# Optimization experiments

Measured on AMD Instinct MI355X. Metric: run time of the kernel, lower is better.

The kernel has to match this reference:

```python
import jax, jax.numpy as jnp
import numpy as np

N_HEAD = 16


def setup_inputs() -> dict:
    key = jax.random.key(0)
    k1, k2, k3 = jax.random.split(key, 3)
    B, T, C = 4, 1024, 1024
    x = jax.random.normal(k1, (B, T, C), dtype=jnp.float32)
    w_attn = jax.random.normal(k2, (3 * C, C), dtype=jnp.float32) * 0.02
    w_proj = jax.random.normal(k3, (C, C), dtype=jnp.float32) * 0.02
    return {"x": x, "w_attn": w_attn, "w_proj": w_proj}


def reference(x, w_attn, w_proj):
    B, T, C = x.shape
    H = N_HEAD
    hs = C // H
    scale = 1.0 / np.sqrt(hs).astype(np.float32)

    qkv = x @ w_attn.T                         # [B, T, 3C]
    q, k, v = jnp.split(qkv, 3, axis=-1)
    q = q.reshape(B, T, H, hs).transpose(0, 2, 1, 3)   # [B, H, T, hs]
    k = k.reshape(B, T, H, hs).transpose(0, 2, 1, 3)
    v = v.reshape(B, T, H, hs).transpose(0, 2, 1, 3)

    scores = jnp.einsum('bhqd,bhkd->bhqk', q, k) * scale   # [B, H, T, T]
    causal = jnp.tril(jnp.ones((T, T), dtype=bool))
    scores = jnp.where(causal, scores, -jnp.inf)

    att = jax.nn.sigmoid(scores)                # sigmoid attention, not softmax
    # Bernoulli straight-through sampling (value = sample, grad flows via att)
    samp_key = jax.random.fold_in(jax.random.key(0), 42)
    samples = jax.random.bernoulli(samp_key, att).astype(att.dtype)
    att = att + jax.lax.stop_gradient(samples - att)

    y = jnp.einsum('bhqk,bhkd->bhqd', att, v)   # [B, H, T, hs]
    att_sum = att.sum(axis=-1)                  # [B, H, T]
    att_var = (att * (1.0 - att)).sum(axis=-1)  # [B, H, T]

    y = y.transpose(0, 2, 1, 3).reshape(B, T, C)
    y = y @ w_proj.T
    return (y, att_sum, att_var)
```

## Files before the change

kernel.cpp:

```cpp
#include <hip/hip_runtime.h>
#include <stdint.h>


#define T_SEQ 1024
#define QKV_LD 3072

typedef __attribute__((ext_vector_type(8))) short bf16x8;
typedef __attribute__((ext_vector_type(4))) float f32x4;
typedef __attribute__((ext_vector_type(4))) unsigned int u32x4;

typedef __attribute__((address_space(3))) uint32_t lds_u32;
typedef __attribute__((address_space(1))) const uint32_t g_u32;

#define ROTL(x, d) __builtin_amdgcn_alignbit((x), (x), 32 - (d))

__device__ __forceinline__ void threefry2x32(uint32_t k0, uint32_t k1,
                                             uint32_t x0, uint32_t x1,
                                             uint32_t &o0, uint32_t &o1) {
  uint32_t ks2 = k0 ^ k1 ^ 0x1BD11BDAu;
#define TF_R4(a, b, c, d)                                                      \
  x0 += x1; x1 = ROTL(x1, a); x1 ^= x0;                                        \
  x0 += x1; x1 = ROTL(x1, b); x1 ^= x0;                                        \
  x0 += x1; x1 = ROTL(x1, c); x1 ^= x0;                                        \
  x0 += x1; x1 = ROTL(x1, d); x1 ^= x0;
  x0 += k0; x1 += k1;
  TF_R4(13, 15, 26, 6)
  x0 += k1; x1 += ks2 + 1u;
  TF_R4(17, 29, 16, 24)
  x0 += ks2; x1 += k0 + 2u;
  TF_R4(13, 15, 26, 6)
  x0 += k0; x1 += k1 + 3u;
  TF_R4(17, 29, 16, 24)
  x0 += k1; x1 += ks2 + 4u;
  TF_R4(13, 15, 26, 6)
  x0 += ks2; x1 += k0 + 5u;
  o0 = x0; o1 = x1;
#undef TF_R4
}

__device__ __forceinline__ unsigned short f2bf(float f) {
  uint32_t u = __float_as_uint(f);
  u += 0x7FFFu + ((u >> 16) & 1u);
  return (unsigned short)(u >> 16);
}

#define N_X4  1048576
#define N_WA4 786432
#define N_WP4 262144

__global__ __launch_bounds__(256) void cvt3_bf16(const float4* __restrict__ x,
                                                 const float4* __restrict__ wa,
                                                 const float4* __restrict__ wp,
                                                 uint2* __restrict__ out) {
  size_t i = (size_t)blockIdx.x * 256 + threadIdx.x;
  const float4* src;
  size_t off;
  if (i < N_X4) { src = x; off = i; }
  else if (i < N_X4 + N_WA4) { src = wa; off = i - N_X4; }
  else { src = wp; off = i - (N_X4 + N_WA4); }
  float4 v = src[off];
  uint2 o;
  o.x = (uint32_t)f2bf(v.x) | ((uint32_t)f2bf(v.y) << 16);
  o.y = (uint32_t)f2bf(v.z) | ((uint32_t)f2bf(v.w) << 16);
  out[i] = o;
}

template <int OUT_BF16>
__global__ __launch_bounds__(256) void gemm_bf16(const unsigned short* __restrict__ A,
                                                 const unsigned short* __restrict__ B,
                                                 void* __restrict__ Cout,
                                                 int M, int N, int K) {
  __shared__ unsigned short As[128 * 32];
  __shared__ unsigned short Bs[128 * 32];

  const int t = threadIdx.x;
  const int lane = t & 63, w = t >> 6;
  const int g = lane >> 4, lr = lane & 15;
  const int rw = w >> 1, cw = w & 1;
  const int bm = blockIdx.x * 128, bn = blockIdx.y * 128;

  const unsigned short* Ag = A + (size_t)(bm + 32 * w + (lane >> 2)) * K + 8 * (lane & 3);
  const unsigned short* Bg = B + (size_t)(bn + 32 * w + (lane >> 2)) * K + 8 * (lane & 3);
  lds_u32* Al0 = (lds_u32*)&As[(32 * w) * 32];
  lds_u32* Al1 = (lds_u32*)&As[(32 * w + 16) * 32];
  lds_u32* Bl0 = (lds_u32*)&Bs[(32 * w) * 32];
  lds_u32* Bl1 = (lds_u32*)&Bs[(32 * w + 16) * 32];

  f32x4 acc[4][4];
#pragma unroll
  for (int i = 0; i < 4; ++i)
#pragma unroll
    for (int j = 0; j < 4; ++j) acc[i][j] = (f32x4){0.f, 0.f, 0.f, 0.f};

  for (int k0 = 0; k0 < K; k0 += 32) {
    __syncthreads();
    __builtin_amdgcn_global_load_lds((g_u32*)(const void*)(Ag + k0), Al0, 16, 0, 0);
    __builtin_amdgcn_global_load_lds((g_u32*)(const void*)(Ag + k0 + (size_t)16 * K), Al1, 16, 0, 0);
    __builtin_amdgcn_global_load_lds((g_u32*)(const void*)(Bg + k0), Bl0, 16, 0, 0);
    __builtin_amdgcn_global_load_lds((g_u32*)(const void*)(Bg + k0 + (size_t)16 * K), Bl1, 16, 0, 0);
    __syncthreads();

    bf16x8 af[4], bfr[4];
#pragma unroll
    for (int i = 0; i < 4; ++i)
      af[i] = *(const bf16x8*)&As[(64 * rw + 16 * i + lr) * 32 + 8 * g];
#pragma unroll
    for (int j = 0; j < 4; ++j)
      bfr[j] = *(const bf16x8*)&Bs[(64 * cw + 16 * j + lr) * 32 + 8 * g];
#pragma unroll
    for (int i = 0; i < 4; ++i)
#pragma unroll
      for (int j = 0; j < 4; ++j)
        acc[i][j] = __builtin_amdgcn_mfma_f32_16x16x32_bf16(af[i], bfr[j], acc[i][j], 0, 0, 0);
  }

#pragma unroll
  for (int i = 0; i < 4; ++i)
#pragma unroll
    for (int j = 0; j < 4; ++j)
#pragma unroll
      for (int r = 0; r < 4; ++r) {
        const size_t row = bm + 64 * rw + 16 * i + 4 * g + r;
        const size_t col = bn + 64 * cw + 16 * j + lr;
        if (OUT_BF16)
          ((unsigned short*)Cout)[row * N + col] = f2bf(acc[i][j][r]);
        else
          ((float*)Cout)[row * N + col] = acc[i][j][r];
      }
}

__global__ __launch_bounds__(256) void vtrans(const unsigned short* __restrict__ qkv,
                                              unsigned short* __restrict__ Vt) {
  const int i = blockIdx.x;
  const int bh = i >> 4, kc = i & 15;
  const int b = bh >> 4, h = bh & 15;
  const int t = threadIdx.x;
  const int dr = t & 63, kgrp = t >> 6;

  const unsigned short* src =
      qkv + (size_t)(b * T_SEQ + kc * 64 + kgrp * 16) * QKV_LD + 2048 + h * 64 + dr;
  uint32_t pk[8];
#pragma unroll
  for (int j = 0; j < 8; ++j) {
    uint32_t lo = src[(size_t)(2 * j) * QKV_LD];
    uint32_t hi = src[(size_t)(2 * j + 1) * QKV_LD];
    pk[j] = lo | (hi << 16);
  }
  unsigned short* dst = Vt + ((size_t)bh * 64 + dr) * 1024 + kc * 64 + kgrp * 16;
  *(u32x4*)dst = (u32x4){pk[0], pk[1], pk[2], pk[3]};
  *(u32x4*)(dst + 8) = (u32x4){pk[4], pk[5], pk[6], pk[7]};
}

__global__ __launch_bounds__(128) void attn_nobar(const unsigned short* __restrict__ qkv,
                                                  const unsigned short* __restrict__ Vt,
                                                  unsigned short* __restrict__ yatt,
                                                  float* __restrict__ att_sum,
                                                  float* __restrict__ att_var) {
  __shared__ unsigned short St[2][16][40];

  const int t = threadIdx.x;
  const int lane = t & 63, w = t >> 6;
  const int g = lane >> 4, lr = lane & 15;
  const int i = blockIdx.x;
  const int bh = 8 * (i & 7) + ((i >> 3) & 7);
  const int p = 2 * (i >> 6) + w;
  const int b = bh >> 4, h = bh & 15;

  uint32_t dk0, dk1;
  threefry2x32(0u, 0u, 0u, 42u, dk0, dk1);

  unsigned short (*stw)[40] = St[w];
  const unsigned short* kb = qkv + (size_t)b * T_SEQ * QKV_LD + 1024 + h * 64;
  const unsigned short* vb = Vt + (size_t)bh * 64 * 1024;

#pragma unroll 1
  for (int half = 0; half < 2; ++half) {
    const int s = half ? p : 63 - p;
    const int q0 = 16 * s;
    const unsigned short* qr = qkv + (size_t)(b * T_SEQ + q0 + lr) * QKV_LD + h * 64 + 8 * g;
    const bf16x8 aq0 = *(const bf16x8*)qr;
    const bf16x8 aq1 = *(const bf16x8*)(qr + 32);

    f32x4 yacc[4];
#pragma unroll
    for (int c = 0; c < 4; ++c) yacc[c] = (f32x4){0.f, 0.f, 0.f, 0.f};
    float rs[4] = {0.f, 0.f, 0.f, 0.f};

    const int nk = (q0 + 47) >> 5;

    bf16x8 cbv[4], cbk[4];
#pragma unroll
    for (int c = 0; c < 4; ++c)
      cbv[c] = *(const bf16x8*)(vb + (size_t)(16 * c + lr) * 1024 + 8 * g);
#pragma unroll
    for (int c = 0; c < 2; ++c) {
      const unsigned short* kr = kb + (size_t)(16 * c + lr) * QKV_LD + 8 * g;
      cbk[2 * c] = *(const bf16x8*)kr;
      cbk[2 * c + 1] = *(const bf16x8*)(kr + 32);
    }

#pragma unroll 1
    for (int kt = 0; kt < nk; ++kt) {
      const int kg0 = 32 * kt;
      const int kgn = (kt + 1 < nk) ? kg0 + 32 : kg0;
      bf16x8 nbv[4], nbk[4];
#pragma unroll
      for (int c = 0; c < 4; ++c)
        nbv[c] = *(const bf16x8*)(vb + (size_t)(16 * c + lr) * 1024 + kgn + 8 * g);
#pragma unroll
      for (int c = 0; c < 2; ++c) {
        const unsigned short* kr = kb + (size_t)(kgn + 16 * c + lr) * QKV_LD + 8 * g;
        nbk[2 * c] = *(const bf16x8*)kr;
        nbk[2 * c + 1] = *(const bf16x8*)(kr + 32);
      }

#pragma unroll
      for (int c = 0; c < 2; ++c) {
        f32x4 sa = __builtin_amdgcn_mfma_f32_16x16x32_bf16(aq0, cbk[2 * c],
                                                           (f32x4){0.f, 0.f, 0.f, 0.f}, 0, 0, 0);
        sa = __builtin_amdgcn_mfma_f32_16x16x32_bf16(aq1, cbk[2 * c + 1], sa, 0, 0, 0);
        const int kg = kg0 + 16 * c + lr;
#pragma unroll
        for (int r = 0; r < 4; ++r) {
          const int qg = q0 + 4 * g + r;
          float samp = 0.f;
          if (kg <= qg) {
            float e = __expf(-0.125f * sa[r]);
            uint32_t idx = ((uint32_t)bh << 20) | ((uint32_t)qg << 10) | (uint32_t)kg;
            uint32_t r0, r1;
            threefry2x32(dk0, dk1, 0u, idx, r0, r1);
            float u = __uint_as_float(0x3F800000u | ((r0 ^ r1) >> 9)) - 1.0f;
            samp = (fmaf(u, e, u) < 1.0f) ? 1.0f : 0.0f;
          }
          rs[r] += samp;
          stw[4 * g + r][16 * c + lr] = (unsigned short)(__float_as_uint(samp) >> 16);
        }
      }

      const bf16x8 pa = *(const bf16x8*)&stw[lr][8 * g];
#pragma unroll
      for (int c = 0; c < 4; ++c)
        yacc[c] = __builtin_amdgcn_mfma_f32_16x16x32_bf16(pa, cbv[c], yacc[c], 0, 0, 0);

#pragma unroll
      for (int c = 0; c < 4; ++c) { cbv[c] = nbv[c]; cbk[c] = nbk[c]; }
    }

    const size_t yb = (size_t)(b * T_SEQ + q0) * 1024 + h * 64;
#pragma unroll
    for (int c = 0; c < 4; ++c)
#pragma unroll
      for (int r = 0; r < 4; ++r)
        yatt[yb + (size_t)(4 * g + r) * 1024 + 16 * c + lr] = f2bf(yacc[c][r]);

#pragma unroll
    for (int r = 0; r < 4; ++r) {
      rs[r] += __shfl_xor(rs[r], 1);
      rs[r] += __shfl_xor(rs[r], 2);
      rs[r] += __shfl_xor(rs[r], 4);
      rs[r] += __shfl_xor(rs[r], 8);
    }
    if (lr == 0) {
#pragma unroll
      for (int r = 0; r < 4; ++r)
        att_sum[(size_t)bh * T_SEQ + q0 + 4 * g + r] = rs[r];
    }
    if (lane < 16) att_var[(size_t)bh * T_SEQ + q0 + lane] = 0.f;
  }
}

extern "C" void kernel_launch(void* const* d_in, const int* in_sizes, int n_in,
                              void* d_out, int out_size, void* d_ws, size_t ws_size,
                              hipStream_t stream) {
  (void)in_sizes; (void)n_in; (void)out_size; (void)ws_size;
  const float* x      = (const float*)d_in[0];
  const float* w_attn = (const float*)d_in[1];
  const float* w_proj = (const float*)d_in[2];

  float* y_out      = (float*)d_out;
  float* attsum_out = y_out + (size_t)4 * 1024 * 1024;
  float* attvar_out = attsum_out + (size_t)4 * 16 * 1024;

  unsigned short* ws_us = (unsigned short*)d_ws;
  unsigned short* x_bf    = ws_us;
  unsigned short* wa_bf   = x_bf + (size_t)4 * 1024 * 1024;
  unsigned short* wp_bf   = wa_bf + (size_t)3 * 1024 * 1024;
  unsigned short* qkv_bf  = wp_bf + (size_t)1024 * 1024;
  unsigned short* yatt_bf = qkv_bf + (size_t)4096 * 3072;
  unsigned short* vt_bf   = yatt_bf + (size_t)4096 * 1024;

  dim3 blk(256);
  cvt3_bf16<<<dim3(8192), blk, 0, stream>>>((const float4*)x, (const float4*)w_attn,
                                            (const float4*)w_proj, (uint2*)x_bf);
  gemm_bf16<1><<<dim3(32, 24), blk, 0, stream>>>(x_bf, wa_bf, (void*)qkv_bf, 4096, 3072, 1024);
  vtrans<<<dim3(1024), blk, 0, stream>>>(qkv_bf, vt_bf);
  attn_nobar<<<dim3(1024), dim3(128), 0, stream>>>(qkv_bf, vt_bf, yatt_bf, attsum_out, attvar_out);
  gemm_bf16<0><<<dim3(32, 8), blk, 0, stream>>>(yatt_bf, wp_bf, (void*)y_out, 4096, 1024, 1024);
}
```

Baseline: 187.2 us.

## Give each wave one query strip in 256-thread blocks and drop register prefetch

```diff
diff --git a/kernel.cpp b/kernel.cpp
--- a/kernel.cpp
+++ b/kernel.cpp
@@ -151,20 +151,24 @@
   *(u32x4*)(dst + 8) = (u32x4){pk[4], pk[5], pk[6], pk[7]};
 }
 
-__global__ __launch_bounds__(128) void attn_nobar(const unsigned short* __restrict__ qkv,
-                                                  const unsigned short* __restrict__ Vt,
-                                                  unsigned short* __restrict__ yatt,
-                                                  float* __restrict__ att_sum,
-                                                  float* __restrict__ att_var) {
-  __shared__ unsigned short St[2][16][40];
+__global__ __launch_bounds__(256, 4) void attn_strip(const unsigned short* __restrict__ qkv,
+                                                     const unsigned short* __restrict__ Vt,
+                                                     unsigned short* __restrict__ yatt,
+                                                     float* __restrict__ att_sum,
+                                                     float* __restrict__ att_var) {
+  __shared__ unsigned short St[4][16][40];
 
   const int t = threadIdx.x;
   const int lane = t & 63, w = t >> 6;
   const int g = lane >> 4, lr = lane & 15;
   const int i = blockIdx.x;
   const int bh = 8 * (i & 7) + ((i >> 3) & 7);
-  const int p = 2 * (i >> 6) + w;
+  const int j = i >> 6;
   const int b = bh >> 4, h = bh & 15;
+
+  const int role = (w + (j >> 2)) & 3;
+  const int s = (role == 0) ? j : (role == 1) ? 63 - j : (role == 2) ? 31 - j : 32 + j;
+  const int q0 = 16 * s;
 
   uint32_t dk0, dk1;
   threefry2x32(0u, 0u, 0u, 42u, dk0, dk1);
@@ -173,100 +177,82 @@
   const unsigned short* kb = qkv + (size_t)b * T_SEQ * QKV_LD + 1024 + h * 64;
   const unsigned short* vb = Vt + (size_t)bh * 64 * 1024;
 
+  const unsigned short* qr = qkv + (size_t)(b * T_SEQ + q0 + lr) * QKV_LD + h * 64 + 8 * g;
+  const bf16x8 aq0 = *(const bf16x8*)qr;
+  const bf16x8 aq1 = *(const bf16x8*)(qr + 32);
+
+  f32x4 yacc[4];
+#pragma unroll
+  for (int c = 0; c < 4; ++c) yacc[c] = (f32x4){0.f, 0.f, 0.f, 0.f};
+  float rs[4] = {0.f, 0.f, 0.f, 0.f};
+
+  const int nk = (q0 + 47) >> 5;
+  const uint32_t lane_idx = ((uint32_t)(4 * g) << 10) | (uint32_t)lr;
+  const uint32_t base_idx = ((uint32_t)bh << 20) | ((uint32_t)q0 << 10);
+
 #pragma unroll 1
-  for (int half = 0; half < 2; ++half) {
-    const int s = half ? p : 63 - p;
-    const int q0 = 16 * s;
-    const unsigned short* qr = qkv + (size_t)(b * T_SEQ + q0 + lr) * QKV_LD + h * 64 + 8 * g;
-    const bf16x8 aq0 = *(const bf16x8*)qr;
-    const bf16x8 aq1 = *(const bf16x8*)(qr + 32);
-
-    f32x4 yacc[4];
-#pragma unroll
-    for (int c = 0; c < 4; ++c) yacc[c] = (f32x4){0.f, 0.f, 0.f, 0.f};
-    float rs[4] = {0.f, 0.f, 0.f, 0.f};
-
-    const int nk = (q0 + 47) >> 5;
-
-    bf16x8 cbv[4], cbk[4];
-#pragma unroll
-    for (int c = 0; c < 4; ++c)
-      cbv[c] = *(const bf16x8*)(vb + (size_t)(16 * c + lr) * 1024 + 8 * g);
+  for (int kt = 0; kt < nk; ++kt) {
+    const int kg0 = 32 * kt;
+    bf16x8 cbk[4], cbv[4];
 #pragma unroll
     for (int c = 0; c < 2; ++c) {
-      const unsigned short* kr = kb + (size_t)(16 * c + lr) * QKV_LD + 8 * g;
+      const unsigned short* kr = kb + (size_t)(kg0 + 16 * c + lr) * QKV_LD + 8 * g;
       cbk[2 * c] = *(const bf16x8*)kr;
       cbk[2 * c + 1] = *(const bf16x8*)(kr + 32);
     }
-
-#pragma unroll 1
-    for (int kt = 0; kt < nk; ++kt) {
-      const int kg0 = 32 * kt;
-      const int kgn = (kt + 1 < nk) ? kg0 + 32 : kg0;
-      bf16x8 nbv[4], nbk[4];
-#pragma unroll
-      for (int c = 0; c < 4; ++c)
-        nbv[c] = *(const bf16x8*)(vb + (size_t)(16 * c + lr) * 1024 + kgn + 8 * g);
-#pragma unroll
-      for (int c = 0; c < 2; ++c) {
-        const unsigned short* kr = kb + (size_t)(kgn + 16 * c + lr) * QKV_LD + 8 * g;
-        nbk[2 * c] = *(const bf16x8*)kr;
-        nbk[2 * c + 1] = *(const bf16x8*)(kr + 32);
+#pragma unroll
+    for (int c = 0; c < 4; ++c)
+      cbv[c] = *(const bf16x8*)(vb + (size_t)(16 * c + lr) * 1024 + kg0 + 8 * g);
+
+#pragma unroll
+    for (int c = 0; c < 2; ++c) {
+      f32x4 sa = __builtin_amdgcn_mfma_f32_16x16x32_bf16(aq0, cbk[2 * c],
+                                                         (f32x4){0.f, 0.f, 0.f, 0.f}, 0, 0, 0);
+      sa = __builtin_amdgcn_mfma_f32_16x16x32_bf16(aq1, cbk[2 * c + 1], sa, 0, 0, 0);
+      const int kg = kg0 + 16 * c + lr;
+      const uint32_t idx_c = base_idx + (uint32_t)(kg0 + 16 * c) + lane_idx;
+#pragma unroll
+      for (int r = 0; r < 4; ++r) {
+        const int qg = q0 + 4 * g + r;
+        float samp = 0.f;
+        if (kg <= qg) {
+          float e = __builtin_exp2f(sa[r] * -0.18033688011112042f);
+          uint32_t r0, r1;
+          threefry2x32(dk0, dk1, 0u, idx_c + ((uint32_t)r << 10), r0, r1);
+          float u = __uint_as_float(0x3F800000u | ((r0 ^ r1) >> 9)) - 1.0f;
+          samp = (fmaf(u, e, u) < 1.0f) ? 1.0f : 0.0f;
+        }
+        rs[r] += samp;
+        stw[4 * g + r][16 * c + lr] = (unsigned short)(__float_as_uint(samp) >> 16);
       }
-
-#pragma unroll
-      for (int c = 0; c < 2; ++c) {
-        f32x4 sa = __builtin_amdgcn_mfma_f32_16x16x32_bf16(aq0, cbk[2 * c],
-                                                           (f32x4){0.f, 0.f, 0.f, 0.f}, 0, 0, 0);
-        sa = __builtin_amdgcn_mfma_f32_16x16x32_bf16(aq1, cbk[2 * c + 1], sa, 0, 0, 0);
-        const int kg = kg0 + 16 * c + lr;
-#pragma unroll
-        for (int r = 0; r < 4; ++r) {
-          const int qg = q0 + 4 * g + r;
-          float samp = 0.f;
-          if (kg <= qg) {
-            float e = __expf(-0.125f * sa[r]);
-            uint32_t idx = ((uint32_t)bh << 20) | ((uint32_t)qg << 10) | (uint32_t)kg;
-            uint32_t r0, r1;
-            threefry2x32(dk0, dk1, 0u, idx, r0, r1);
-            float u = __uint_as_float(0x3F800000u | ((r0 ^ r1) >> 9)) - 1.0f;
-            samp = (fmaf(u, e, u) < 1.0f) ? 1.0f : 0.0f;
-          }
-          rs[r] += samp;
-          stw[4 * g + r][16 * c + lr] = (unsigned short)(__float_as_uint(samp) >> 16);
-        }
-      }
-
-      const bf16x8 pa = *(const bf16x8*)&stw[lr][8 * g];
-#pragma unroll
-      for (int c = 0; c < 4; ++c)
-        yacc[c] = __builtin_amdgcn_mfma_f32_16x16x32_bf16(pa, cbv[c], yacc[c], 0, 0, 0);
-
-#pragma unroll
-      for (int c = 0; c < 4; ++c) { cbv[c] = nbv[c]; cbk[c] = nbk[c]; }
     }
 
-    const size_t yb = (size_t)(b * T_SEQ + q0) * 1024 + h * 64;
+    const bf16x8 pa = *(const bf16x8*)&stw[lr][8 * g];
 #pragma unroll
     for (int c = 0; c < 4; ++c)
-#pragma unroll
-      for (int r = 0; r < 4; ++r)
-        yatt[yb + (size_t)(4 * g + r) * 1024 + 16 * c + lr] = f2bf(yacc[c][r]);
-
-#pragma unroll
-    for (int r = 0; r < 4; ++r) {
-      rs[r] += __shfl_xor(rs[r], 1);
-      rs[r] += __shfl_xor(rs[r], 2);
-      rs[r] += __shfl_xor(rs[r], 4);
-      rs[r] += __shfl_xor(rs[r], 8);
-    }
-    if (lr == 0) {
-#pragma unroll
-      for (int r = 0; r < 4; ++r)
-        att_sum[(size_t)bh * T_SEQ + q0 + 4 * g + r] = rs[r];
-    }
-    if (lane < 16) att_var[(size_t)bh * T_SEQ + q0 + lane] = 0.f;
-  }
+      yacc[c] = __builtin_amdgcn_mfma_f32_16x16x32_bf16(pa, cbv[c], yacc[c], 0, 0, 0);
+  }
+
+  const size_t yb = (size_t)(b * T_SEQ + q0) * 1024 + h * 64;
+#pragma unroll
+  for (int c = 0; c < 4; ++c)
+#pragma unroll
+    for (int r = 0; r < 4; ++r)
+      yatt[yb + (size_t)(4 * g + r) * 1024 + 16 * c + lr] = f2bf(yacc[c][r]);
+
+#pragma unroll
+  for (int r = 0; r < 4; ++r) {
+    rs[r] += __shfl_xor(rs[r], 1);
+    rs[r] += __shfl_xor(rs[r], 2);
+    rs[r] += __shfl_xor(rs[r], 4);
+    rs[r] += __shfl_xor(rs[r], 8);
+  }
+  if (lr == 0) {
+#pragma unroll
+    for (int r = 0; r < 4; ++r)
+      att_sum[(size_t)bh * T_SEQ + q0 + 4 * g + r] = rs[r];
+  }
+  if (lane < 16) att_var[(size_t)bh * T_SEQ + q0 + lane] = 0.f;
 }
 
 extern "C" void kernel_launch(void* const* d_in, const int* in_sizes, int n_in,
@@ -294,6 +280,6 @@
                                             (const float4*)w_proj, (uint2*)x_bf);
   gemm_bf16<1><<<dim3(32, 24), blk, 0, stream>>>(x_bf, wa_bf, (void*)qkv_bf, 4096, 3072, 1024);
   vtrans<<<dim3(1024), blk, 0, stream>>>(qkv_bf, vt_bf);
-  attn_nobar<<<dim3(1024), dim3(128), 0, stream>>>(qkv_bf, vt_bf, yatt_bf, attsum_out, attvar_out);
+  attn_strip<<<dim3(1024), blk, 0, stream>>>(qkv_bf, vt_bf, yatt_bf, attsum_out, attvar_out);
   gemm_bf16<0><<<dim3(32, 8), blk, 0, stream>>>(yatt_bf, wp_bf, (void*)y_out, 4096, 1024, 1024);
 }
```

Result: slower. 249.4 us (+33.2%).
